# Kernel tuning notes

Hardware: AMD Instinct MI355X
Metric: run time of the kernel (lower is better)

The kernel has to match this reference:

```python
import jax, jax.numpy as jnp
import numpy as np

N = 8192
D = 512

def _row_normalize(m):
    # row-normalize; rows summing to 0 get inverse 0 (inf -> 0 in original)
    rs = m.sum(axis=1, keepdims=True)
    inv = jnp.where(rs == 0, 0.0, 1.0 / rs)
    return m * inv

def setup_inputs() -> dict:
    key = jax.random.key(0)
    k1, k2 = jax.random.split(key)
    qf = jax.random.normal(k1, (N, D), dtype=jnp.float32)
    gf = jax.random.normal(k2, (N, D), dtype=jnp.float32)
    return {"qf": qf, "gf": gf}

def reference(qf, gf):
    # feature = row-normalized squared difference  [N, D]
    feature = _row_normalize((qf - gf) ** 2)
    # adj[i, j] = ||feature_i - feature_j||^2, via GEMM expansion
    sq = jnp.sum(feature * feature, axis=-1)                  # [N]
    adj = sq[:, None] + sq[None, :] - 2.0 * (feature @ feature.T)  # [N, N]
    # symmetrize: elementwise max(adj, adj.T) (equivalent to the masked mix)
    adj = jnp.maximum(adj, adj.T)
    # add identity and row-normalize
    adj = adj + jnp.eye(N, dtype=adj.dtype)
    adj = _row_normalize(adj)
    return adj, feature
```

## Files before the change

kernel.cpp:

```cpp
#include <hip/hip_runtime.h>
#include <hip/hip_bf16.h>

#define N 8192
#define D 512

typedef __attribute__((ext_vector_type(8))) short short8;
typedef __attribute__((ext_vector_type(4))) float f32x4;

__device__ __forceinline__ float block_reduce_256(float v, float* red) {
    #pragma unroll
    for (int o = 1; o < 64; o <<= 1) v += __shfl_xor(v, o, 64);
    int w = threadIdx.x >> 6;
    if ((threadIdx.x & 63) == 0) red[w] = v;
    __syncthreads();
    float tot = red[0] + red[1] + red[2] + red[3];
    __syncthreads();
    return tot;
}

__global__ void feature_kernel(const float* __restrict__ qf, const float* __restrict__ gf,
                               float* __restrict__ feat, __hip_bfloat16* __restrict__ featb,
                               float* __restrict__ sq) {
    __shared__ float red[4];
    int row = blockIdx.x, t = threadIdx.x;
    const float2* q2 = (const float2*)(qf + (size_t)row * D);
    const float2* g2 = (const float2*)(gf + (size_t)row * D);
    float2 qv = q2[t], gv = g2[t];
    float a = qv.x - gv.x, b = qv.y - gv.y;
    float va = a * a, vb = b * b;
    float rs = block_reduce_256(va + vb, red);
    float inv = (rs == 0.0f) ? 0.0f : 1.0f / rs;
    float fa = va * inv, fb = vb * inv;
    ((float2*)(feat + (size_t)row * D))[t] = make_float2(fa, fb);
    __hip_bfloat162 h;
    h.x = __float2bfloat16(fa);
    h.y = __float2bfloat16(fb);
    ((__hip_bfloat162*)(featb + (size_t)row * D))[t] = h;
    float tot = block_reduce_256(fa * fa + fb * fb, red);
    if (t == 0) sq[row] = tot;
}

__global__ void colsum_partial_kernel(const float* __restrict__ feat, float* __restrict__ partial) {
    int b = blockIdx.x, t = threadIdx.x;
    const float* fp = feat + (size_t)b * 128 * D;
    float a0 = 0.f, a1 = 0.f;
    for (int r = 0; r < 128; ++r) {
        a0 += fp[r * D + t];
        a1 += fp[r * D + t + 256];
    }
    partial[b * D + t] = a0;
    partial[b * D + t + 256] = a1;
}

__global__ void finalize_kernel(const float* __restrict__ partial, const float* __restrict__ sq,
                                float* __restrict__ cvec, float* __restrict__ Sval) {
    __shared__ float red[4];
    int t = threadIdx.x;
    if (blockIdx.x == 0) {
        float a0 = 0.f, a1 = 0.f;
        for (int b = 0; b < 64; ++b) {
            a0 += partial[b * D + t];
            a1 += partial[b * D + t + 256];
        }
        cvec[t] = a0;
        cvec[t + 256] = a1;
    } else {
        float s = 0.f;
        for (int k = 0; k < N / 256; ++k) s += sq[t + 256 * k];
        float tot = block_reduce_256(s, red);
        if (t == 0) Sval[0] = tot;
    }
}

__global__ void rowinv_kernel(const float* __restrict__ feat, const float* __restrict__ sq,
                              const float* __restrict__ cvec, const float* __restrict__ Sval,
                              float* __restrict__ rowinv) {
    __shared__ float red[4];
    int row = blockIdx.x, t = threadIdx.x;
    float2 f = ((const float2*)(feat + (size_t)row * D))[t];
    float2 c = ((const float2*)cvec)[t];
    float dot = block_reduce_256(f.x * c.x + f.y * c.y, red);
    if (t == 0) {
        float rs = (float)N * sq[row] + Sval[0] - 2.0f * dot + 1.0f;
        rowinv[row] = (rs == 0.0f) ? 0.0f : 1.0f / rs;
    }
}

__global__ __launch_bounds__(256, 2) void adj_gemm_sym_kernel(const __hip_bfloat16* __restrict__ featb,
                                                              const float* __restrict__ sq,
                                                              const float* __restrict__ rowinv,
                                                              float* __restrict__ out) {
    __shared__ __align__(16) char lds[73728];
    int wg = blockIdx.x;
    int id = (wg & 7) * 260 + (wg >> 3);
    int r = (int)((129.0f - sqrtf(16641.0f - 8.0f * (float)id)) * 0.5f);
    if (r > 63) r = 63;
    while (r > 0 && (r * (129 - r)) / 2 > id) --r;
    while (((r + 1) * (128 - r)) / 2 <= id) ++r;
    int by = r;
    int bx = r + (id - (r * (129 - r)) / 2);
    int rowBase = by * 128, colBase = bx * 128;

    int t = threadIdx.x, lane = t & 63, w = t >> 6;
    int wr = w >> 1, wc = w & 1, g = lane >> 4;

    f32x4 acc[4][4];
    #pragma unroll
    for (int m = 0; m < 4; ++m)
        #pragma unroll
        for (int n = 0; n < 4; ++n) acc[m][n] = (f32x4){0.f, 0.f, 0.f, 0.f};

    int srow = t >> 3, schunk = t & 7;
    const __hip_bfloat16* gA = featb + (size_t)(rowBase + srow) * D + schunk * 8;
    const __hip_bfloat16* gB = featb + (size_t)(colBase + srow) * D + schunk * 8;
    int wo0 = srow * 128 + ((schunk ^ (srow & 7)) * 16);

    int arow = wr * 64 + (lane & 15);
    int brow = wc * 64 + (lane & 15);
    int swzc = lane & 7;

    short8 ra[4], rb[4];
    #pragma unroll
    for (int q = 0; q < 4; ++q) {
        ra[q] = *(const short8*)(gA + (size_t)q * 32 * D);
        rb[q] = *(const short8*)(gB + (size_t)q * 32 * D);
    }
    #pragma unroll
    for (int q = 0; q < 4; ++q) {
        *(short8*)(lds + wo0 + q * 4096) = ra[q];
        *(short8*)(lds + 32768 + wo0 + q * 4096) = rb[q];
    }
    __syncthreads();

    int cur = 0;
    for (int ks = 0; ks < 8; ++ks) {
        if (ks < 7) {
            int k0 = (ks + 1) * 64;
            #pragma unroll
            for (int q = 0; q < 4; ++q) {
                ra[q] = *(const short8*)(gA + (size_t)q * 32 * D + k0);
                rb[q] = *(const short8*)(gB + (size_t)q * 32 * D + k0);
            }
        }
        const char* pA = lds + (cur << 14);
        const char* pB = lds + 32768 + (cur << 14);
        #pragma unroll
        for (int kk = 0; kk < 2; ++kk) {
            int ca = ((kk * 4 + g) ^ swzc) * 16;
            short8 af[4], bf[4];
            #pragma unroll
            for (int m = 0; m < 4; ++m) {
                af[m] = *(const short8*)(pA + (arow + 16 * m) * 128 + ca);
                bf[m] = *(const short8*)(pB + (brow + 16 * m) * 128 + ca);
            }
            #pragma unroll
            for (int m = 0; m < 4; ++m)
                #pragma unroll
                for (int n = 0; n < 4; ++n)
                    acc[m][n] = __builtin_amdgcn_mfma_f32_16x16x32_bf16(af[m], bf[n], acc[m][n], 0, 0, 0);
        }
        if (ks < 7) {
            char* wA = lds + ((cur ^ 1) << 14);
            char* wB = lds + 32768 + ((cur ^ 1) << 14);
            #pragma unroll
            for (int q = 0; q < 4; ++q) {
                *(short8*)(wA + wo0 + q * 4096) = ra[q];
                *(short8*)(wB + wo0 + q * 4096) = rb[q];
            }
        }
        __syncthreads();
        cur ^= 1;
    }

    float* T = (float*)(lds + w * 18432);
    float sqj[4];
    int jcol[4];
    #pragma unroll
    for (int n = 0; n < 4; ++n) {
        jcol[n] = colBase + wc * 64 + n * 16 + (lane & 15);
        sqj[n] = sq[jcol[n]];
    }
    int offdiag = (by != bx);
    #pragma unroll
    for (int m = 0; m < 4; ++m) {
        int ibase = rowBase + wr * 64 + m * 16 + g * 4;
        #pragma unroll
        for (int rI = 0; rI < 4; ++rI) {
            int i = ibase + rI;
            float si = sq[i], ri = rowinv[i];
            size_t ro = (size_t)i * N;
            #pragma unroll
            for (int n = 0; n < 4; ++n) {
                float pre = si + sqj[n] - 2.0f * acc[m][n][rI] + (i == jcol[n] ? 1.0f : 0.0f);
                out[ro + jcol[n]] = pre * ri;
                if (offdiag) {
                    int ii = m * 16 + g * 4 + rI;
                    int jj = n * 16 + (lane & 15);
                    T[jj * 72 + ii] = pre;
                }
            }
        }
    }
    if (offdiag) {
        __syncthreads();
        #pragma unroll
        for (int it = 0; it < 16; ++it) {
            int jj = it * 4 + g;
            int ii0 = (lane & 15) * 4;
            f32x4 v = *(const f32x4*)&T[jj * 72 + ii0];
            int j = colBase + wc * 64 + jj;
            float rj = rowinv[j];
            v *= rj;
            *(f32x4*)&out[(size_t)j * N + rowBase + wr * 64 + ii0] = v;
        }
    }
}

extern "C" void kernel_launch(void* const* d_in, const int* in_sizes, int n_in,
                              void* d_out, int out_size, void* d_ws, size_t ws_size,
                              hipStream_t stream) {
    const float* qf = (const float*)d_in[0];
    const float* gf = (const float*)d_in[1];
    float* out = (float*)d_out;
    float* feat = out + (size_t)N * N;

    char* wsb = (char*)d_ws;
    __hip_bfloat16* featb = (__hip_bfloat16*)wsb;
    float* sq      = (float*)(wsb + 8388608);
    float* partial = (float*)(wsb + 8388608 + 32768);
    float* cvec    = (float*)(wsb + 8388608 + 32768 + 131072);
    float* Sval    = (float*)(wsb + 8388608 + 32768 + 131072 + 2048);
    float* rowinv  = (float*)(wsb + 8388608 + 32768 + 131072 + 2048 + 64);

    feature_kernel<<<N, 256, 0, stream>>>(qf, gf, feat, featb, sq);
    colsum_partial_kernel<<<64, 256, 0, stream>>>(feat, partial);
    finalize_kernel<<<2, 256, 0, stream>>>(partial, sq, cvec, Sval);
    rowinv_kernel<<<N, 256, 0, stream>>>(feat, sq, cvec, Sval, rowinv);
    adj_gemm_sym_kernel<<<2080, 256, 0, stream>>>(featb, sq, rowinv, out);
}
```

Baseline: 125.1 us.

## Compute full adjacency with 256x256 tiles instead of symmetric half plus transpose

Replaces the upper-triangular 128x128 tiling, which wrote each off-diagonal tile twice via an LDS transpose, with a full 32x32 grid of 256x256 tiles run by 512-thread workgroups. Each block now writes only its own tile with coalesced row stores. It drops the transpose staging and the triangular index math, but redoes about twice the GEMM FLOPs. It also raises per-thread accumulator count and LDS usage to 128KB. Output stays exactly symmetric because the GEMM is symmetric per element.

```diff
diff --git a/kernel.cpp b/kernel.cpp
--- a/kernel.cpp
+++ b/kernel.cpp
@@ -86,49 +86,44 @@
     }
 }
 
-__global__ __launch_bounds__(256, 2) void adj_gemm_sym_kernel(const __hip_bfloat16* __restrict__ featb,
-                                                              const float* __restrict__ sq,
-                                                              const float* __restrict__ rowinv,
-                                                              float* __restrict__ out) {
-    __shared__ __align__(16) char lds[73728];
+__global__ __launch_bounds__(512, 2) void adj_gemm_kernel(const __hip_bfloat16* __restrict__ featb,
+                                                          const float* __restrict__ sq,
+                                                          const float* __restrict__ rowinv,
+                                                          float* __restrict__ out) {
+    __shared__ __align__(16) char lds[131072];
     int wg = blockIdx.x;
-    int id = (wg & 7) * 260 + (wg >> 3);
-    int r = (int)((129.0f - sqrtf(16641.0f - 8.0f * (float)id)) * 0.5f);
-    if (r > 63) r = 63;
-    while (r > 0 && (r * (129 - r)) / 2 > id) --r;
-    while (((r + 1) * (128 - r)) / 2 <= id) ++r;
-    int by = r;
-    int bx = r + (id - (r * (129 - r)) / 2);
-    int rowBase = by * 128, colBase = bx * 128;
+    int id = (wg & 7) * 128 + (wg >> 3);
+    int bx = id & 31, by = id >> 5;
+    int rowBase = by * 256, colBase = bx * 256;
 
     int t = threadIdx.x, lane = t & 63, w = t >> 6;
-    int wr = w >> 1, wc = w & 1, g = lane >> 4;
-
-    f32x4 acc[4][4];
-    #pragma unroll
-    for (int m = 0; m < 4; ++m)
+    int wr = w >> 2, wc = w & 3, g = lane >> 4;
+
+    f32x4 acc[8][4];
+    #pragma unroll
+    for (int m = 0; m < 8; ++m)
         #pragma unroll
         for (int n = 0; n < 4; ++n) acc[m][n] = (f32x4){0.f, 0.f, 0.f, 0.f};
 
-    int srow = t >> 3, schunk = t & 7;
-    const __hip_bfloat16* gA = featb + (size_t)(rowBase + srow) * D + schunk * 8;
-    const __hip_bfloat16* gB = featb + (size_t)(colBase + srow) * D + schunk * 8;
-    int wo0 = srow * 128 + ((schunk ^ (srow & 7)) * 16);
-
-    int arow = wr * 64 + (lane & 15);
+    int srow = t >> 3, scol = t & 7;
+    const __hip_bfloat16* gA = featb + (size_t)(rowBase + srow) * D + scol * 8;
+    const __hip_bfloat16* gB = featb + (size_t)(colBase + srow) * D + scol * 8;
+    int wo0 = srow * 128 + ((scol ^ (srow & 7)) * 16);
+
+    int arow = wr * 128 + (lane & 15);
     int brow = wc * 64 + (lane & 15);
     int swzc = lane & 7;
 
     short8 ra[4], rb[4];
     #pragma unroll
     for (int q = 0; q < 4; ++q) {
-        ra[q] = *(const short8*)(gA + (size_t)q * 32 * D);
-        rb[q] = *(const short8*)(gB + (size_t)q * 32 * D);
+        ra[q] = *(const short8*)(gA + (size_t)q * 64 * D);
+        rb[q] = *(const short8*)(gB + (size_t)q * 64 * D);
     }
     #pragma unroll
     for (int q = 0; q < 4; ++q) {
-        *(short8*)(lds + wo0 + q * 4096) = ra[q];
-        *(short8*)(lds + 32768 + wo0 + q * 4096) = rb[q];
+        *(short8*)(lds + wo0 + q * 8192) = ra[q];
+        *(short8*)(lds + 65536 + wo0 + q * 8192) = rb[q];
     }
     __syncthreads();
 
@@ -138,41 +133,40 @@
             int k0 = (ks + 1) * 64;
             #pragma unroll
             for (int q = 0; q < 4; ++q) {
-                ra[q] = *(const short8*)(gA + (size_t)q * 32 * D + k0);
-                rb[q] = *(const short8*)(gB + (size_t)q * 32 * D + k0);
-            }
-        }
-        const char* pA = lds + (cur << 14);
-        const char* pB = lds + 32768 + (cur << 14);
+                ra[q] = *(const short8*)(gA + (size_t)q * 64 * D + k0);
+                rb[q] = *(const short8*)(gB + (size_t)q * 64 * D + k0);
+            }
+        }
+        const char* pA = lds + cur * 32768;
+        const char* pB = lds + 65536 + cur * 32768;
         #pragma unroll
         for (int kk = 0; kk < 2; ++kk) {
             int ca = ((kk * 4 + g) ^ swzc) * 16;
-            short8 af[4], bf[4];
-            #pragma unroll
-            for (int m = 0; m < 4; ++m) {
-                af[m] = *(const short8*)(pA + (arow + 16 * m) * 128 + ca);
-                bf[m] = *(const short8*)(pB + (brow + 16 * m) * 128 + ca);
-            }
-            #pragma unroll
-            for (int m = 0; m < 4; ++m)
+            short8 bf[4];
+            #pragma unroll
+            for (int n = 0; n < 4; ++n)
+                bf[n] = *(const short8*)(pB + (brow + 16 * n) * 128 + ca);
+            #pragma unroll
+            for (int m = 0; m < 8; ++m) {
+                short8 af = *(const short8*)(pA + (arow + 16 * m) * 128 + ca);
                 #pragma unroll
                 for (int n = 0; n < 4; ++n)
-                    acc[m][n] = __builtin_amdgcn_mfma_f32_16x16x32_bf16(af[m], bf[n], acc[m][n], 0, 0, 0);
+                    acc[m][n] = __builtin_amdgcn_mfma_f32_16x16x32_bf16(af, bf[n], acc[m][n], 0, 0, 0);
+            }
         }
         if (ks < 7) {
-            char* wA = lds + ((cur ^ 1) << 14);
-            char* wB = lds + 32768 + ((cur ^ 1) << 14);
+            char* wA = lds + (cur ^ 1) * 32768;
+            char* wB = lds + 65536 + (cur ^ 1) * 32768;
             #pragma unroll
             for (int q = 0; q < 4; ++q) {
-                *(short8*)(wA + wo0 + q * 4096) = ra[q];
-                *(short8*)(wB + wo0 + q * 4096) = rb[q];
+                *(short8*)(wA + wo0 + q * 8192) = ra[q];
+                *(short8*)(wB + wo0 + q * 8192) = rb[q];
             }
         }
         __syncthreads();
         cur ^= 1;
     }
 
-    float* T = (float*)(lds + w * 18432);
     float sqj[4];
     int jcol[4];
     #pragma unroll
@@ -180,10 +174,9 @@
         jcol[n] = colBase + wc * 64 + n * 16 + (lane & 15);
         sqj[n] = sq[jcol[n]];
     }
-    int offdiag = (by != bx);
-    #pragma unroll
-    for (int m = 0; m < 4; ++m) {
-        int ibase = rowBase + wr * 64 + m * 16 + g * 4;
+    #pragma unroll
+    for (int m = 0; m < 8; ++m) {
+        int ibase = rowBase + wr * 128 + m * 16 + g * 4;
         #pragma unroll
         for (int rI = 0; rI < 4; ++rI) {
             int i = ibase + rI;
@@ -193,25 +186,7 @@
             for (int n = 0; n < 4; ++n) {
                 float pre = si + sqj[n] - 2.0f * acc[m][n][rI] + (i == jcol[n] ? 1.0f : 0.0f);
                 out[ro + jcol[n]] = pre * ri;
-                if (offdiag) {
-                    int ii = m * 16 + g * 4 + rI;
-                    int jj = n * 16 + (lane & 15);
-                    T[jj * 72 + ii] = pre;
-                }
-            }
-        }
-    }
-    if (offdiag) {
-        __syncthreads();
-        #pragma unroll
-        for (int it = 0; it < 16; ++it) {
-            int jj = it * 4 + g;
-            int ii0 = (lane & 15) * 4;
-            f32x4 v = *(const f32x4*)&T[jj * 72 + ii0];
-            int j = colBase + wc * 64 + jj;
-            float rj = rowinv[j];
-            v *= rj;
-            *(f32x4*)&out[(size_t)j * N + rowBase + wr * 64 + ii0] = v;
+            }
         }
     }
 }
@@ -236,5 +211,5 @@
     colsum_partial_kernel<<<64, 256, 0, stream>>>(feat, partial);
     finalize_kernel<<<2, 256, 0, stream>>>(partial, sq, cvec, Sval);
     rowinv_kernel<<<N, 256, 0, stream>>>(feat, sq, cvec, Sval, rowinv);
-    adj_gemm_sym_kernel<<<2080, 256, 0, stream>>>(featb, sq, rowinv, out);
-}
+    adj_gemm_kernel<<<1024, 512, 0, stream>>>(featb, sq, rowinv, out);
+}
```

After: 135.0 us. +7.9%, slower.
